# Optimization experiments

Measured on AMD Instinct MI355X. Metric: run time of the kernel, lower is better.

Reference implementation:

```python
import jax, jax.numpy as jnp
import numpy as np

D_MODEL = 1024
NUM_HEADS = 16
HEAD_DIM = D_MODEL // NUM_HEADS  # 64
ROPE_THETA = 10000.0
SEQ_LEN = 4096
BATCH = 1


def apply_rope(x, positions, theta=ROPE_THETA):
    # x: [b, h, s, d], positions: [s]
    d = x.shape[-1]
    inv_freq = theta ** (-jnp.arange(0, d, 2, dtype=jnp.float32) / d)  # [d/2]
    angles = positions.astype(jnp.float32)[:, None] * inv_freq[None, :]  # [s, d/2]
    cos = jnp.cos(angles)  # [s, d/2]
    sin = jnp.sin(angles)
    x1 = x[..., 0::2]  # [b, h, s, d/2]
    x2 = x[..., 1::2]
    r1 = x1 * cos - x2 * sin
    r2 = x1 * sin + x2 * cos
    # interleave back to [..., d]
    out = jnp.stack([r1, r2], axis=-1).reshape(x.shape)
    return out.astype(x.dtype)


def setup_inputs() -> dict:
    key = jax.random.key(0)
    k_x, k_qkv, k_o = jax.random.split(key, 3)
    scale_in = 1.0 / np.sqrt(D_MODEL)
    return {
        "x": jax.random.normal(k_x, (BATCH, SEQ_LEN, D_MODEL), dtype=jnp.float32),
        "token_positions": jnp.arange(SEQ_LEN, dtype=jnp.int64 if jax.config.jax_enable_x64 else jnp.int32),
        "w_qkv": jax.random.normal(k_qkv, (3 * D_MODEL, D_MODEL), dtype=jnp.float32) * scale_in,
        "w_o": jax.random.normal(k_o, (D_MODEL, D_MODEL), dtype=jnp.float32) * scale_in,
    }


def reference(x, token_positions, w_qkv, w_o):
    b, s, _ = x.shape
    # QKV projection (Linear without bias, weight [out, in])
    x_qkv = jnp.einsum('bsd,ed->bse', x, w_qkv)  # [b, s, 3*d_model]
    # rearrange 'b s (three heads kv) -> three b heads s kv'
    x_qkv = x_qkv.reshape(b, s, 3, NUM_HEADS, HEAD_DIM)
    x_qkv = jnp.transpose(x_qkv, (2, 0, 3, 1, 4))  # [3, b, h, s, d]
    q, k, v = x_qkv[0], x_qkv[1], x_qkv[2]
    q = apply_rope(q, token_positions)
    k = apply_rope(k, token_positions)
    # scaled dot-product attention with causal mask
    scores = jnp.einsum('bhnd,bhmd->bhnm', q, k) / jnp.sqrt(jnp.float32(HEAD_DIM))
    causal = jnp.tril(jnp.ones((s, s), dtype=bool))  # [s, s]
    scores = jnp.where(causal[None, None], scores, jnp.float32(-jnp.inf))
    weights = jax.nn.softmax(scores, axis=-1)
    attn = jnp.einsum('bhnm,bhmd->bhnd', weights, v)  # [b, h, s, d]
    attn = jnp.transpose(attn, (0, 2, 1, 3)).reshape(b, s, NUM_HEADS * HEAD_DIM)
    return jnp.einsum('bsd,ed->bse', attn, w_o)
```

## Files before the change

### kernel.cpp

```cpp
#include <hip/hip_runtime.h>

#define SEQ 4096
#define DMODEL 1024
#define HEADS 16
#define HD 64
#define NQKV 3072

typedef __attribute__((ext_vector_type(8))) __bf16 bf16x8;
typedef __attribute__((ext_vector_type(4))) __bf16 bf16x4;
typedef __attribute__((ext_vector_type(8))) short short8;
typedef __attribute__((ext_vector_type(4))) float f32x4;
typedef __attribute__((ext_vector_type(16))) float f32x16;
typedef __attribute__((ext_vector_type(4))) unsigned int u32x4;

__device__ __forceinline__ unsigned short f2bf(float f) {
    unsigned u = __builtin_bit_cast(unsigned, f);
    return (unsigned short)((u + 0x7fffu + ((u >> 16) & 1u)) >> 16);
}
__device__ __forceinline__ float bf2f(unsigned short h) {
    return __builtin_bit_cast(float, (unsigned)h << 16);
}
__device__ __forceinline__ unsigned cvt_pk_bf16(float lo, float hi) {
    unsigned r;
    asm("v_cvt_pk_bf16_f32 %0, %1, %2" : "=v"(r) : "v"(lo), "v"(hi));
    return r;
}

__device__ __forceinline__ void gload16(const void* g, void* l) {
    __builtin_amdgcn_global_load_lds(
        (const __attribute__((address_space(1))) unsigned int*)g,
        (__attribute__((address_space(3))) unsigned int*)l, 16, 0, 0);
}

#define TS(qt, kh) (0x40 | ((kh) << 5) | (qt))
__device__ __constant__ unsigned char TASKS[28] = {
    TS(15,0), TS(15,1), TS(14,0), TS(14,1), TS(13,0), TS(13,1),
    TS(12,0), TS(12,1), TS(11,0), TS(11,1), TS(10,0), TS(10,1),
    TS(9,0),  TS(9,1),  TS(8,0),  TS(8,1),  TS(7,0),  TS(7,1),
    3,        TS(6,0),  TS(6,1),  2,        TS(5,0),  TS(5,1),
    TS(4,0),  TS(4,1),  1,        0
};

__global__ void f2bf_all(const float* __restrict__ x, const float* __restrict__ wqkv,
                         const float* __restrict__ wo, const int* __restrict__ pos,
                         unsigned short* __restrict__ dst,
                         float* __restrict__ csT, float* __restrict__ snT) {
    const int N0 = SEQ * DMODEL / 4;
    const int N1 = N0 + NQKV * DMODEL / 4;
    const int NT = N1 + DMODEL * DMODEL / 4;
    int i = blockIdx.x * 256 + threadIdx.x;
    int stride = gridDim.x * 256;
    for (; i < NT; i += stride) {
        const float4* src;
        if (i < N0)      src = reinterpret_cast<const float4*>(x) + i;
        else if (i < N1) src = reinterpret_cast<const float4*>(wqkv) + (i - N0);
        else             src = reinterpret_cast<const float4*>(wo) + (i - N1);
        float4 f = *src;
        ushort4 o;
        o.x = f2bf(f.x); o.y = f2bf(f.y); o.z = f2bf(f.z); o.w = f2bf(f.w);
        reinterpret_cast<ushort4*>(dst)[i] = o;
    }
    const float kk = -13.287712379549449f / 32.0f;
    for (int idx = blockIdx.x * 256 + threadIdx.x; idx < SEQ * 32; idx += stride) {
        int s = idx >> 5, fi = idx & 31;
        float p = (float)pos[s];
        float ang = p * exp2f((float)fi * kk);
        float sn_, cs_;
        sincosf(ang, &sn_, &cs_);
        csT[idx] = cs_;
        snT[idx] = sn_;
    }
}

__global__ __launch_bounds__(256) void gemm_qkv(const unsigned short* __restrict__ A,
                                                const unsigned short* __restrict__ B,
                                                unsigned short* __restrict__ outB,
                                                unsigned short* __restrict__ vtp,
                                                const float* __restrict__ csT,
                                                const float* __restrict__ snT,
                                                int M, int N, int K) {
    alignas(16) __shared__ unsigned short a_lds[2][128 * 32];
    alignas(16) __shared__ unsigned short b_lds[2][128 * 32];
    __shared__ unsigned short vtile[4][16][72];
    const int tid = threadIdx.x;
    const int wave = tid >> 6, lane = tid & 63;
    const int l16 = lane & 15, g = lane >> 4;
    const int wr = wave >> 1, wc = wave & 1;

    const int bid = blockIdx.x;
    const int t = (bid & 7) * 96 + (bid >> 3);
    const int bm = t / 24, bn = t % 24;

    const int lrow = lane >> 2;
    const int lcol = (lane & 3) * 8;

    const unsigned short* Ag = A + (size_t)(bm * 128 + lrow) * K + lcol;
    const unsigned short* Bg = B + (size_t)(bn * 128 + lrow) * K + lcol;

    f32x4 acc[4][4] = {};
    const int NS = K / 32;

    auto STAGE = [&](int b, int ks) {
#pragma unroll
        for (int j = 0; j < 2; ++j) {
            int chunk = wave * 2 + j;
            gload16(Ag + (size_t)(chunk * 16) * K + ks * 32, a_lds[b] + chunk * 512);
            gload16(Bg + (size_t)(chunk * 16) * K + ks * 32, b_lds[b] + chunk * 512);
        }
    };

    STAGE(0, 0);

    for (int ks = 0; ks < NS; ++ks) {
        const int cur = ks & 1;
        asm volatile("s_waitcnt vmcnt(0)" ::: "memory");
        __builtin_amdgcn_s_barrier();
        if (ks + 1 < NS) STAGE(cur ^ 1, ks + 1);

        bf16x8 af[4], bfr[4];
#pragma unroll
        for (int m = 0; m < 4; ++m)
            af[m] = *reinterpret_cast<const bf16x8*>(a_lds[cur] + (wr * 64 + m * 16 + l16) * 32 + g * 8);
#pragma unroll
        for (int n = 0; n < 4; ++n)
            bfr[n] = *reinterpret_cast<const bf16x8*>(b_lds[cur] + (wc * 64 + n * 16 + l16) * 32 + g * 8);
        __builtin_amdgcn_s_setprio(1);
#pragma unroll
        for (int m = 0; m < 4; ++m)
#pragma unroll
            for (int n = 0; n < 4; ++n)
                acc[m][n] = __builtin_amdgcn_mfma_f32_16x16x32_bf16(af[m], bfr[n], acc[m][n], 0, 0, 0);
        __builtin_amdgcn_s_setprio(0);
    }

    const float QS = 0.125f * 1.4426950408889634f;
#pragma unroll
    for (int n = 0; n < 4; ++n) {
        const int col = bn * 128 + wc * 64 + n * 16 + l16;
        const int part = col >> 10;
        const int hh = (col >> 6) & 15;
        if (part < 2) {
            const int fi = (col & 63) >> 1;
            const float sc = (part == 0) ? QS : 1.0f;
            const bool odd = (col & 1) != 0;
#pragma unroll
            for (int m = 0; m < 4; ++m)
#pragma unroll
                for (int r = 0; r < 4; ++r) {
                    int row = bm * 128 + wr * 64 + m * 16 + g * 4 + r;
                    float v = acc[m][n][r];
                    float pp = __shfl_xor(v, 1);
                    float cs_ = csT[row * 32 + fi];
                    float sn_ = snT[row * 32 + fi];
                    float out = odd ? (pp * sn_ + v * cs_) : (v * cs_ - pp * sn_);
                    outB[(size_t)((part * HEADS + hh) * SEQ + row) * HD + (col & 63)] = f2bf(out * sc);
                }
        } else {
#pragma unroll
            for (int m = 0; m < 4; ++m)
#pragma unroll
                for (int r = 0; r < 4; ++r)
                    vtile[wave][l16][m * 16 + g * 4 + r] = f2bf(acc[m][n][r]);
#pragma unroll
            for (int dd = 0; dd < 16; ++dd) {
                int dg = ((col & 63) & ~15) + dd;
                vtp[(size_t)(hh * HD + dg) * SEQ + bm * 128 + wr * 64 + lane] =
                    vtile[wave][dd][lane];
            }
        }
    }
}

__global__ __launch_bounds__(256) void gemm_out(const unsigned short* __restrict__ A,
                                                const unsigned short* __restrict__ B,
                                                float* __restrict__ outF,
                                                int M, int N, int K) {
    alignas(16) __shared__ unsigned short a_lds[2][128 * 32];
    alignas(16) __shared__ unsigned short b_lds[2][64 * 32];
    const int tid = threadIdx.x;
    const int wave = tid >> 6, lane = tid & 63;
    const int l16 = lane & 15, g = lane >> 4;
    const int wr = wave >> 1, wc = wave & 1;
    const int bm = blockIdx.x, bn = blockIdx.y;

    const int lrow = lane >> 2;
    const int lcol = (lane & 3) * 8;

    const unsigned short* Ag = A + (size_t)(bm * 128 + lrow) * K + lcol;
    const unsigned short* Bg = B + (size_t)(bn * 64 + lrow) * K + lcol;

    f32x4 acc[4][2] = {};
    const int NS = K / 32;

    auto STAGE = [&](int b, int ks) {
#pragma unroll
        for (int j = 0; j < 2; ++j) {
            int chunk = wave * 2 + j;
            gload16(Ag + (size_t)(chunk * 16) * K + ks * 32, a_lds[b] + chunk * 512);
        }
        gload16(Bg + (size_t)(wave * 16) * K + ks * 32, b_lds[b] + wave * 512);
    };

    STAGE(0, 0);

    for (int ks = 0; ks < NS; ++ks) {
        const int cur = ks & 1;
        asm volatile("s_waitcnt vmcnt(0)" ::: "memory");
        __builtin_amdgcn_s_barrier();
        if (ks + 1 < NS) STAGE(cur ^ 1, ks + 1);

        bf16x8 af[4], bfr[2];
#pragma unroll
        for (int m = 0; m < 4; ++m)
            af[m] = *reinterpret_cast<const bf16x8*>(a_lds[cur] + (wr * 64 + m * 16 + l16) * 32 + g * 8);
#pragma unroll
        for (int n = 0; n < 2; ++n)
            bfr[n] = *reinterpret_cast<const bf16x8*>(b_lds[cur] + (wc * 32 + n * 16 + l16) * 32 + g * 8);
        __builtin_amdgcn_s_setprio(1);
#pragma unroll
        for (int m = 0; m < 4; ++m)
#pragma unroll
            for (int n = 0; n < 2; ++n)
                acc[m][n] = __builtin_amdgcn_mfma_f32_16x16x32_bf16(af[m], bfr[n], acc[m][n], 0, 0, 0);
        __builtin_amdgcn_s_setprio(0);
    }

#pragma unroll
    for (int m = 0; m < 4; ++m)
#pragma unroll
        for (int n = 0; n < 2; ++n)
#pragma unroll
            for (int r = 0; r < 4; ++r) {
                int row = bm * 128 + wr * 64 + m * 16 + g * 4 + r;
                int col = bn * 64 + wc * 32 + n * 16 + l16;
                outF[(size_t)row * N + col] = acc[m][n][r];
            }
}

__global__ __launch_bounds__(512) void attn_kernel(const unsigned short* __restrict__ qkv,
                                                   const unsigned short* __restrict__ vt,
                                                   unsigned short* __restrict__ attnout,
                                                   int* __restrict__ qcnt,
                                                   unsigned short* __restrict__ pO,
                                                   float* __restrict__ lmf) {
    const int xcd = blockIdx.x & 7;
    const int tid = threadIdx.x;
    const int wave = tid >> 6, lane = tid & 63;
    const int l32 = lane & 31, hi = lane >> 5;

    alignas(16) __shared__ unsigned short k_lds[2][128 * 64];
    alignas(16) __shared__ unsigned short v_lds[2][2][64 * 64];
    __shared__ int slot_sh;

    const int rsw = (l32 & 7) << 4;

    for (;;) {
        if (tid == 0) slot_sh = atomicAdd(&qcnt[xcd], 1);
        __syncthreads();
        const int t = slot_sh;
        __syncthreads();
        if (t >= 56) break;

        const int hloc = t & 1;
        const unsigned char e = TASKS[t >> 1];
        const int qtile = e & 31;
        const int khalf = (e >> 5) & 1;
        const bool isSplit = (e >> 6) != 0;
        const int T = 2 * qtile + 2, Hh = qtile + 1;
        const int k0 = isSplit ? (khalf ? Hh : 0) : 0;
        const int k1 = isSplit ? (khalf ? T : Hh) : T;
        const int h = xcd * 2 + hloc;

        const unsigned short* Qg = qkv + (size_t)((0 * HEADS + h) * SEQ) * HD;
        const unsigned short* Kg = qkv + (size_t)((1 * HEADS + h) * SEQ) * HD;
        const unsigned short* VTg = vt + (size_t)h * HD * SEQ;

        const int qbase = qtile * 256 + wave * 32;
        const int qrow = qbase + l32;

        bf16x8 qf[4];
#pragma unroll
        for (int dg = 0; dg < 4; ++dg)
            qf[dg] = *reinterpret_cast<const bf16x8*>(Qg + (size_t)qrow * HD + dg * 16 + hi * 8);

        f32x16 oa[2] = {};
        float m_r = -1e30f, l_r = 0.f;

        auto STAGE = [&](int b, int kt) {
#pragma unroll
            for (int i = 0; i < 2; ++i) {
                int base = wave * 2048 + i * 1024;
                int byte = base + lane * 16;
                int krow = byte >> 7;
                int kc8 = ((byte >> 4) & 7) ^ (krow & 7);
                gload16(Kg + (size_t)(kt * 128 + krow) * HD + kc8 * 8, (char*)k_lds[b] + base);
                int fr = byte >> 7;
                int h64 = fr >> 6, vd = fr & 63;
                int vc8 = ((byte >> 4) & 7) ^ (vd & 7);
                gload16(VTg + (size_t)vd * SEQ + kt * 128 + h64 * 64 + vc8 * 8,
                        (char*)v_lds[b] + base);
            }
        };

        STAGE(0, k0);

        for (int kt = k0; kt < k1; ++kt) {
            const int cur = (kt - k0) & 1;
            asm volatile("s_waitcnt vmcnt(0)" ::: "memory");
            __builtin_amdgcn_s_barrier();
            if (kt + 1 < k1) STAGE(cur ^ 1, kt + 1);

#pragma unroll
            for (int hh = 0; hh < 2; ++hh) {
                if (hh && (kt * 128 + 64) > (qbase + 31)) break;

                f32x16 s[2] = {};
                __builtin_amdgcn_s_setprio(1);
#pragma unroll
                for (int g = 0; g < 2; ++g) {
                    int row = hh * 64 + g * 32 + l32;
#pragma unroll
                    for (int dg = 0; dg < 4; ++dg) {
                        bf16x8 kf = *reinterpret_cast<const bf16x8*>(
                            (char*)k_lds[cur] + row * 128 + ((dg * 32 + hi * 16) ^ rsw));
                        s[g] = __builtin_amdgcn_mfma_f32_32x32x16_bf16(kf, qf[dg], s[g], 0, 0, 0);
                    }
                }
                __builtin_amdgcn_s_setprio(0);

                if (kt * 128 + hh * 64 + 63 > qbase) {
#pragma unroll
                    for (int g = 0; g < 2; ++g)
#pragma unroll
                        for (int r = 0; r < 16; ++r) {
                            int kv = kt * 128 + hh * 64 + g * 32 + (r & 3) + 8 * (r >> 2) + 4 * hi;
                            if (kv > qrow) s[g][r] = -1e30f;
                        }
                }

                float ma = -1e30f, mb = -1e30f, mc = -1e30f, md = -1e30f;
#pragma unroll
                for (int r = 0; r < 16; r += 4) {
                    ma = fmaxf(ma, fmaxf(s[0][r], s[1][r]));
                    mb = fmaxf(mb, fmaxf(s[0][r + 1], s[1][r + 1]));
                    mc = fmaxf(mc, fmaxf(s[0][r + 2], s[1][r + 2]));
                    md = fmaxf(md, fmaxf(s[0][r + 3], s[1][r + 3]));
                }
                float mx = fmaxf(fmaxf(ma, mb), fmaxf(mc, md));
                mx = fmaxf(mx, __shfl_xor(mx, 32));

                if (__any(mx > m_r + 8.0f)) {
                    float mnew = fmaxf(m_r, mx);
                    float alpha = __builtin_amdgcn_exp2f(m_r - mnew);
                    m_r = mnew;
#pragma unroll
                    for (int r = 0; r < 16; ++r) { oa[0][r] *= alpha; oa[1][r] *= alpha; }
                    l_r *= alpha;
                }

#pragma unroll
                for (int g = 0; g < 2; ++g)
#pragma unroll
                    for (int r = 0; r < 16; ++r) s[g][r] = __builtin_amdgcn_exp2f(s[g][r] - m_r);

                float ra = 0.f, rb = 0.f;
#pragma unroll
                for (int r = 0; r < 16; r += 2) {
                    ra += s[0][r] + s[1][r];
                    rb += s[0][r + 1] + s[1][r + 1];
                }
                float rs = ra + rb;
                rs += __shfl_xor(rs, 32);
                l_r += rs;

                __builtin_amdgcn_s_setprio(1);
#pragma unroll
                for (int g = 0; g < 2; ++g) {
                    u32x4 pfw[2];
#pragma unroll
                    for (int u = 0; u < 2; ++u) {
                        unsigned wA = cvt_pk_bf16(s[g][8 * u + 0], s[g][8 * u + 1]);
                        unsigned wC = cvt_pk_bf16(s[g][8 * u + 2], s[g][8 * u + 3]);
                        unsigned wB = cvt_pk_bf16(s[g][8 * u + 4], s[g][8 * u + 5]);
                        unsigned wD = cvt_pk_bf16(s[g][8 * u + 6], s[g][8 * u + 7]);
                        unsigned wAx = __shfl_xor((int)wA, 32), wBx = __shfl_xor((int)wB, 32);
                        unsigned wCx = __shfl_xor((int)wC, 32), wDx = __shfl_xor((int)wD, 32);
                        pfw[u][0] = hi ? wBx : wA;
                        pfw[u][1] = hi ? wDx : wC;
                        pfw[u][2] = hi ? wB : wAx;
                        pfw[u][3] = hi ? wD : wCx;
                    }
#pragma unroll
                    for (int u = 0; u < 2; ++u) {
                        bf16x8 pf = __builtin_bit_cast(bf16x8, pfw[u]);
                        int ks = g * 2 + u;
#pragma unroll
                        for (int dg = 0; dg < 2; ++dg) {
                            bf16x8 vf = *reinterpret_cast<const bf16x8*>(
                                (char*)v_lds[cur][hh] + (dg * 32 + l32) * 128 + ((ks * 32 + hi * 16) ^ rsw));
                            oa[dg] = __builtin_amdgcn_mfma_f32_32x32x16_bf16(vf, pf, oa[dg], 0, 0, 0);
                        }
                    }
                }
                __builtin_amdgcn_s_setprio(0);
            }
        }

        const int ql = wave * 32 + l32;
        if (isSplit) {
            int sidx = (h * 12 + (qtile - 4)) * 2 + khalf;
            unsigned short* Op = pO + (size_t)sidx * 16384;
#pragma unroll
            for (int dg = 0; dg < 2; ++dg)
#pragma unroll
                for (int rq = 0; rq < 4; ++rq) {
                    ushort4 ov;
                    ov.x = f2bf(oa[dg][4 * rq + 0]);
                    ov.y = f2bf(oa[dg][4 * rq + 1]);
                    ov.z = f2bf(oa[dg][4 * rq + 2]);
                    ov.w = f2bf(oa[dg][4 * rq + 3]);
                    *reinterpret_cast<ushort4*>(Op + ql * 64 + dg * 32 + 8 * rq + 4 * hi) = ov;
                }
            if (hi == 0) {
                lmf[sidx * 512 + ql] = l_r;
                lmf[sidx * 512 + 256 + ql] = m_r;
            }
        } else {
            float inv = 1.0f / l_r;
            unsigned short* orow = attnout + (size_t)(qtile * 256 + ql) * DMODEL + h * HD;
#pragma unroll
            for (int dg = 0; dg < 2; ++dg)
#pragma unroll
                for (int rq = 0; rq < 4; ++rq) {
                    ushort4 ov;
                    ov.x = f2bf(oa[dg][4 * rq + 0] * inv);
                    ov.y = f2bf(oa[dg][4 * rq + 1] * inv);
                    ov.z = f2bf(oa[dg][4 * rq + 2] * inv);
                    ov.w = f2bf(oa[dg][4 * rq + 3] * inv);
                    *reinterpret_cast<ushort4*>(orow + dg * 32 + 8 * rq + 4 * hi) = ov;
                }
        }
    }
}

__global__ __launch_bounds__(256) void merge_kernel(const unsigned short* __restrict__ pO,
                                                    const float* __restrict__ lmf,
                                                    unsigned short* __restrict__ attnout) {
    int idx = blockIdx.x * 256 + threadIdx.x;
    if (idx >= 16 * 12 * 2048) return;
    int h = idx / (12 * 2048);
    int r = idx % (12 * 2048);
    int qt = r >> 11;
    int rr = r & 2047;
    int q = rr >> 3, d8 = rr & 7;

    int s0 = (h * 12 + qt) * 2;
    float l0 = lmf[s0 * 512 + q],       m0 = lmf[s0 * 512 + 256 + q];
    float l1 = lmf[(s0 + 1) * 512 + q], m1 = lmf[(s0 + 1) * 512 + 256 + q];
    float m = fmaxf(m0, m1);
    float a0 = __builtin_amdgcn_exp2f(m0 - m), a1 = __builtin_amdgcn_exp2f(m1 - m);
    float L = l0 * a0 + l1 * a1;
    float c0 = a0 / L, c1 = a1 / L;

    const unsigned short* O0 = pO + (size_t)s0 * 16384 + q * 64 + d8 * 8;
    const unsigned short* O1 = O0 + 16384;
    short8 v0 = *reinterpret_cast<const short8*>(O0);
    short8 v1 = *reinterpret_cast<const short8*>(O1);
    short8 o;
#pragma unroll
    for (int j = 0; j < 8; ++j) {
        float val = bf2f((unsigned short)v0[j]) * c0 + bf2f((unsigned short)v1[j]) * c1;
        o[j] = (short)f2bf(val);
    }
    int qtile = qt + 4;
    *reinterpret_cast<short8*>(attnout + (size_t)(qtile * 256 + q) * DMODEL + h * HD + d8 * 8) = o;
}

extern "C" void kernel_launch(void* const* d_in, const int* in_sizes, int n_in,
                              void* d_out, int out_size, void* d_ws, size_t ws_size,
                              hipStream_t stream) {
    const float* x = (const float*)d_in[0];
    const int* pos = (const int*)d_in[1];
    const float* wqkv = (const float*)d_in[2];
    const float* wo = (const float*)d_in[3];
    float* out = (float*)d_out;

    unsigned short* xb = (unsigned short*)d_ws;
    unsigned short* wqkvb = xb + (size_t)SEQ * DMODEL;
    unsigned short* wob = wqkvb + (size_t)NQKV * DMODEL;
    unsigned short* qkvp = wob + (size_t)DMODEL * DMODEL;
    unsigned short* vtp = qkvp + (size_t)2 * HEADS * SEQ * HD;
    float* csT = (float*)(qkvp + (size_t)3 * HEADS * SEQ * HD);
    float* snT = csT + SEQ * 32;
    unsigned short* attnb = (unsigned short*)(snT + SEQ * 32);

    char* sbase = (char*)d_ws;
    int* qcnt = (int*)sbase;
    float* lmf = (float*)(sbase + 1024);
    unsigned short* pO = (unsigned short*)(sbase + (1 << 20));

    f2bf_all<<<2048, 256, 0, stream>>>(x, wqkv, wo, pos, xb, csT, snT);

    gemm_qkv<<<768, 256, 0, stream>>>(xb, wqkvb, qkvp, vtp, csT, snT, SEQ, NQKV, DMODEL);

    hipMemsetAsync(qcnt, 0, 64, stream);
    attn_kernel<<<512, 512, 0, stream>>>(qkvp, vtp, attnb, qcnt, pO, lmf);
    merge_kernel<<<(16 * 12 * 2048 + 255) / 256, 256, 0, stream>>>(pO, lmf, attnb);

    dim3 g2(SEQ / 128, DMODEL / 64);
    gemm_out<<<g2, 256, 0, stream>>>(attnb, wob, out, SEQ, DMODEL, DMODEL);
}
```

Baseline: 137.1 us.

## Rebalance attention split-K schedule with four-way splits for the longest query tiles

The attention work list is rebuilt: query tiles 14-15 are split into four KV chunks, tiles 5-13 into two, and tiles 0-4 run unsplit, with a new slot mapping and a merge kernel that combines a variable number of partials. The aim is to shorten the critical path of the longest tasks and even out load across the eight per-XCD work queues. Separately, the counter reset moves from a hipMemsetAsync into the first kernel, removing one launch, and 32-row sub-blocks lying entirely above the causal diagonal now skip their QK MFMAs. The price is more partial outputs to write and merge, plus a relocated workspace layout.

```diff
diff --git a/kernel.cpp b/kernel.cpp
--- a/kernel.cpp
+++ b/kernel.cpp
@@ -32,24 +32,28 @@
         (__attribute__((address_space(3))) unsigned int*)l, 16, 0, 0);
 }
 
-#define TS(qt, kh) (0x40 | ((kh) << 5) | (qt))
-__device__ __constant__ unsigned char TASKS[28] = {
-    TS(15,0), TS(15,1), TS(14,0), TS(14,1), TS(13,0), TS(13,1),
-    TS(12,0), TS(12,1), TS(11,0), TS(11,1), TS(10,0), TS(10,1),
-    TS(9,0),  TS(9,1),  TS(8,0),  TS(8,1),  TS(7,0),  TS(7,1),
-    3,        TS(6,0),  TS(6,1),  2,        TS(5,0),  TS(5,1),
-    TS(4,0),  TS(4,1),  1,        0
+#define T2(qt, p) (0x80 | ((p) << 5) | (qt))
+__device__ __constant__ unsigned char TASKS[31] = {
+    T2(15,0), T2(15,1), T2(15,2), T2(15,3),
+    T2(13,0), T2(13,1), T2(14,0), T2(14,1),
+    T2(12,0), T2(12,1), T2(14,2), T2(14,3),
+    T2(11,0), T2(11,1), T2(10,0), T2(10,1),
+    T2(9,0),  T2(9,1),  T2(8,0),  T2(8,1),
+    T2(7,0),  T2(7,1),  4,        T2(6,0),
+    T2(6,1),  T2(5,0),  T2(5,1),  3, 2, 1, 0
 };
 
 __global__ void f2bf_all(const float* __restrict__ x, const float* __restrict__ wqkv,
                          const float* __restrict__ wo, const int* __restrict__ pos,
                          unsigned short* __restrict__ dst,
-                         float* __restrict__ csT, float* __restrict__ snT) {
+                         float* __restrict__ csT, float* __restrict__ snT,
+                         int* __restrict__ qcnt) {
     const int N0 = SEQ * DMODEL / 4;
     const int N1 = N0 + NQKV * DMODEL / 4;
     const int NT = N1 + DMODEL * DMODEL / 4;
     int i = blockIdx.x * 256 + threadIdx.x;
     int stride = gridDim.x * 256;
+    if (blockIdx.x == 0 && threadIdx.x < 16) qcnt[threadIdx.x] = 0;
     for (; i < NT; i += stride) {
         const float4* src;
         if (i < N0)      src = reinterpret_cast<const float4*>(x) + i;
@@ -237,6 +241,11 @@
             }
 }
 
+__device__ __forceinline__ int slot_of(int qt, int p) {
+    if (qt <= 13) return (qt - 5) * 2 + p;
+    return 18 + (qt - 14) * 4 + p;
+}
+
 __global__ __launch_bounds__(512) void attn_kernel(const unsigned short* __restrict__ qkv,
                                                    const unsigned short* __restrict__ vt,
                                                    unsigned short* __restrict__ attnout,
@@ -259,16 +268,23 @@
         __syncthreads();
         const int t = slot_sh;
         __syncthreads();
-        if (t >= 56) break;
+        if (t >= 62) break;
 
         const int hloc = t & 1;
         const unsigned char e = TASKS[t >> 1];
         const int qtile = e & 31;
-        const int khalf = (e >> 5) & 1;
-        const bool isSplit = (e >> 6) != 0;
-        const int T = 2 * qtile + 2, Hh = qtile + 1;
-        const int k0 = isSplit ? (khalf ? Hh : 0) : 0;
-        const int k1 = isSplit ? (khalf ? T : Hh) : T;
+        const int piece = (e >> 5) & 3;
+        const bool isSplit = (e & 0x80) != 0;
+        const int T = 2 * qtile + 2;
+        int k0, k1;
+        if (!isSplit) { k0 = 0; k1 = T; }
+        else if (qtile <= 13) {
+            int Hh = (T + 1) >> 1;
+            k0 = piece ? Hh : 0; k1 = piece ? T : Hh;
+        } else {
+            int ch = (T + 3) >> 2;
+            k0 = piece * ch; k1 = min(T, k0 + ch);
+        }
         const int h = xcd * 2 + hloc;
 
         const unsigned short* Qg = qkv + (size_t)((0 * HEADS + h) * SEQ) * HD;
@@ -318,6 +334,7 @@
                 __builtin_amdgcn_s_setprio(1);
 #pragma unroll
                 for (int g = 0; g < 2; ++g) {
+                    if (kt * 128 + hh * 64 + g * 32 > qbase + 31) continue;
                     int row = hh * 64 + g * 32 + l32;
 #pragma unroll
                     for (int dg = 0; dg < 4; ++dg) {
@@ -408,7 +425,7 @@
 
         const int ql = wave * 32 + l32;
         if (isSplit) {
-            int sidx = (h * 12 + (qtile - 4)) * 2 + khalf;
+            int sidx = h * 26 + slot_of(qtile, piece);
             unsigned short* Op = pO + (size_t)sidx * 16384;
 #pragma unroll
             for (int dg = 0; dg < 2; ++dg)
@@ -447,32 +464,40 @@
                                                     const float* __restrict__ lmf,
                                                     unsigned short* __restrict__ attnout) {
     int idx = blockIdx.x * 256 + threadIdx.x;
-    if (idx >= 16 * 12 * 2048) return;
-    int h = idx / (12 * 2048);
-    int r = idx % (12 * 2048);
-    int qt = r >> 11;
+    if (idx >= 16 * 11 * 2048) return;
+    int h = idx / (11 * 2048);
+    int r = idx % (11 * 2048);
+    int qti = r >> 11;
     int rr = r & 2047;
     int q = rr >> 3, d8 = rr & 7;
-
-    int s0 = (h * 12 + qt) * 2;
-    float l0 = lmf[s0 * 512 + q],       m0 = lmf[s0 * 512 + 256 + q];
-    float l1 = lmf[(s0 + 1) * 512 + q], m1 = lmf[(s0 + 1) * 512 + 256 + q];
-    float m = fmaxf(m0, m1);
-    float a0 = __builtin_amdgcn_exp2f(m0 - m), a1 = __builtin_amdgcn_exp2f(m1 - m);
-    float L = l0 * a0 + l1 * a1;
-    float c0 = a0 / L, c1 = a1 / L;
-
-    const unsigned short* O0 = pO + (size_t)s0 * 16384 + q * 64 + d8 * 8;
-    const unsigned short* O1 = O0 + 16384;
-    short8 v0 = *reinterpret_cast<const short8*>(O0);
-    short8 v1 = *reinterpret_cast<const short8*>(O1);
+    int qtile = qti + 5;
+    int np = (qtile >= 14) ? 4 : 2;
+    int s0 = h * 26 + slot_of(qtile, 0);
+
+    float m = -1e30f;
+#pragma unroll 4
+    for (int p = 0; p < np; ++p) m = fmaxf(m, lmf[(s0 + p) * 512 + 256 + q]);
+    float L = 0.f, c[4];
+#pragma unroll 4
+    for (int p = 0; p < np; ++p) {
+        float lp = lmf[(s0 + p) * 512 + q];
+        float mp = lmf[(s0 + p) * 512 + 256 + q];
+        c[p] = __builtin_amdgcn_exp2f(mp - m);
+        L += lp * c[p];
+    }
+    float invL = 1.0f / L;
+
+    float accv[8] = {};
+#pragma unroll 4
+    for (int p = 0; p < np; ++p) {
+        short8 v = *reinterpret_cast<const short8*>(pO + (size_t)(s0 + p) * 16384 + q * 64 + d8 * 8);
+        float w = c[p] * invL;
+#pragma unroll
+        for (int j = 0; j < 8; ++j) accv[j] += bf2f((unsigned short)v[j]) * w;
+    }
     short8 o;
 #pragma unroll
-    for (int j = 0; j < 8; ++j) {
-        float val = bf2f((unsigned short)v0[j]) * c0 + bf2f((unsigned short)v1[j]) * c1;
-        o[j] = (short)f2bf(val);
-    }
-    int qtile = qt + 4;
+    for (int j = 0; j < 8; ++j) o[j] = (short)f2bf(accv[j]);
     *reinterpret_cast<short8*>(attnout + (size_t)(qtile * 256 + q) * DMODEL + h * HD + d8 * 8) = o;
 }
 
@@ -493,19 +518,18 @@
     float* csT = (float*)(qkvp + (size_t)3 * HEADS * SEQ * HD);
     float* snT = csT + SEQ * 32;
     unsigned short* attnb = (unsigned short*)(snT + SEQ * 32);
+    int* qcnt = (int*)(attnb + (size_t)SEQ * DMODEL);
 
     char* sbase = (char*)d_ws;
-    int* qcnt = (int*)sbase;
-    float* lmf = (float*)(sbase + 1024);
-    unsigned short* pO = (unsigned short*)(sbase + (1 << 20));
-
-    f2bf_all<<<2048, 256, 0, stream>>>(x, wqkv, wo, pos, xb, csT, snT);
+    unsigned short* pO = (unsigned short*)sbase;
+    float* lmf = (float*)(sbase + (size_t)416 * 32768);
+
+    f2bf_all<<<2048, 256, 0, stream>>>(x, wqkv, wo, pos, xb, csT, snT, qcnt);
 
     gemm_qkv<<<768, 256, 0, stream>>>(xb, wqkvb, qkvp, vtp, csT, snT, SEQ, NQKV, DMODEL);
 
-    hipMemsetAsync(qcnt, 0, 64, stream);
     attn_kernel<<<512, 512, 0, stream>>>(qkvp, vtp, attnb, qcnt, pO, lmf);
-    merge_kernel<<<(16 * 12 * 2048 + 255) / 256, 256, 0, stream>>>(pO, lmf, attnb);
+    merge_kernel<<<(16 * 11 * 2048 + 255) / 256, 256, 0, stream>>>(pO, lmf, attnb);
 
     dim3 g2(SEQ / 128, DMODEL / 64);
     gemm_out<<<g2, 256, 0, stream>>>(attnb, wob, out, SEQ, DMODEL, DMODEL);
```

After: 146.9 us. 1.07x slower.
